# Performance work log

Measured on AMD Instinct MI355X. Metric: run time of the kernel, lower is better.

The kernel has to match this reference:

```python
import jax, jax.numpy as jnp
import numpy as np

HIDDEN = 2048
NUM_HEADS = 16
HEAD_DIM = HIDDEN // NUM_HEADS
BATCH, SEQ = 2, 2048


def setup_inputs() -> dict:
    key = jax.random.key(0)
    ks = jax.random.split(key, 9)
    s = 1.0 / np.sqrt(HIDDEN)
    return {
        "hidden_state": jax.random.normal(ks[0], (BATCH, SEQ, HIDDEN), dtype=jnp.float32),
        "Wq": jax.random.normal(ks[1], (HIDDEN, HIDDEN), dtype=jnp.float32) * s,
        "bq": jax.random.normal(ks[2], (HIDDEN,), dtype=jnp.float32) * 0.01,
        "Wk": jax.random.normal(ks[3], (HIDDEN, HIDDEN), dtype=jnp.float32) * s,
        "bk": jax.random.normal(ks[4], (HIDDEN,), dtype=jnp.float32) * 0.01,
        "Wv": jax.random.normal(ks[5], (HIDDEN, HIDDEN), dtype=jnp.float32) * s,
        "bv": jax.random.normal(ks[6], (HIDDEN,), dtype=jnp.float32) * 0.01,
        "Wo": jax.random.normal(ks[7], (HIDDEN, HIDDEN), dtype=jnp.float32) * s,
        "bo": jax.random.normal(ks[8], (HIDDEN,), dtype=jnp.float32) * 0.01,
    }


def _split_heads(x):
    # (B, S, H*D) -> (B, H, S, D)
    b, s, _ = x.shape
    return x.reshape(b, s, NUM_HEADS, HEAD_DIM).transpose(0, 2, 1, 3)


def reference(hidden_state, Wq, bq, Wk, bk, Wv, bv, Wo, bo):
    q = _split_heads(hidden_state @ Wq + bq)
    k = _split_heads(hidden_state @ Wk + bk)
    v = _split_heads(hidden_state @ Wv + bv)
    scale = 1.0 / jnp.sqrt(jnp.asarray(HEAD_DIM, dtype=hidden_state.dtype))
    scores = jnp.einsum("bhqd,bhkd->bhqk", q, k) * scale  # (B,H,S,S)
    probs = jax.nn.softmax(scores, axis=-1)
    out = jnp.einsum("bhqk,bhkd->bhqd", probs, v)  # (B,H,S,D)
    b, h, s, d = out.shape
    out = out.transpose(0, 2, 1, 3).reshape(b, s, h * d)  # merge heads
    return out @ Wo + bo
```

## Files before the change

### kernel.cpp

```cpp
#include <hip/hip_runtime.h>
#include <math.h>

typedef __bf16 bf16;
typedef __bf16 bf16x4 __attribute__((ext_vector_type(4)));
typedef __bf16 bf16x8 __attribute__((ext_vector_type(8)));
typedef float  f32x4  __attribute__((ext_vector_type(4)));

#define HIDDEN 2048
#define NH     16
#define HD     128
#define BATCH  2
#define SEQ    2048
#define MROWS  (BATCH*SEQ)
#define NQKV   (3*HIDDEN)

__device__ __forceinline__ void async16(const bf16* g, bf16* l) {
  __builtin_amdgcn_global_load_lds(
      (const __attribute__((address_space(1))) void*)g,
      (__attribute__((address_space(3))) void*)l, 16, 0, 0);
}

__global__ __launch_bounds__(256) void cast_f32_bf16_kernel(
    const float* __restrict__ src, bf16* __restrict__ dst, int n4) {
  int i = blockIdx.x * 256 + threadIdx.x;
  if (i >= n4) return;
  float4 f = ((const float4*)src)[i];
  bf16x4 o;
  o[0] = (bf16)f.x; o[1] = (bf16)f.y; o[2] = (bf16)f.z; o[3] = (bf16)f.w;
  ((bf16x4*)dst)[i] = o;
}

__global__ __launch_bounds__(256) void transpose_cast4_kernel(
    const float* __restrict__ s0, const float* __restrict__ s1,
    const float* __restrict__ s2, const float* __restrict__ s3,
    bf16* __restrict__ d0, bf16* __restrict__ d1,
    bf16* __restrict__ d2, bf16* __restrict__ d3) {
  const float* src; bf16* dst;
  switch (blockIdx.z) {
    case 0: src = s0; dst = d0; break;
    case 1: src = s1; dst = d1; break;
    case 2: src = s2; dst = d2; break;
    default: src = s3; dst = d3; break;
  }
  __shared__ float t[32][33];
  int x  = blockIdx.x * 32 + threadIdx.x;
  int y0 = blockIdx.y * 32;
#pragma unroll
  for (int i = 0; i < 32; i += 8)
    t[threadIdx.y + i][threadIdx.x] = src[(size_t)(y0 + threadIdx.y + i) * HIDDEN + x];
  __syncthreads();
  int xo  = blockIdx.y * 32 + threadIdx.x;
  int yo0 = blockIdx.x * 32;
#pragma unroll
  for (int i = 0; i < 32; i += 8)
    dst[(size_t)(yo0 + threadIdx.y + i) * HIDDEN + xo] = (bf16)t[threadIdx.x][threadIdx.y + i];
}

__global__ __launch_bounds__(256) void concat3_kernel(
    const float* __restrict__ a, const float* __restrict__ b,
    const float* __restrict__ c, float* __restrict__ dst) {
  int i = blockIdx.x * 256 + threadIdx.x;
  float v = (i < 2048) ? a[i] : (i < 4096 ? b[i - 2048] : c[i - 4096]);
  dst[i] = v;
}

__global__ __launch_bounds__(256) void transpose_v_kernel(
    const bf16* __restrict__ QKV, bf16* __restrict__ Vt) {
  __shared__ bf16 t[32][33];
  int bh = blockIdx.z, b = bh >> 4, h = bh & 15;
  const bf16* src = QKV + (size_t)b * SEQ * NQKV + 2 * HIDDEN + h * HD;
  bf16* dst = Vt + (size_t)bh * HD * SEQ;
  int s0 = blockIdx.x * 32, d0 = blockIdx.y * 32;
#pragma unroll
  for (int i = 0; i < 32; i += 8)
    t[threadIdx.y + i][threadIdx.x] = src[(size_t)(s0 + threadIdx.y + i) * NQKV + d0 + threadIdx.x];
  __syncthreads();
#pragma unroll
  for (int i = 0; i < 32; i += 8)
    dst[(size_t)(d0 + threadIdx.y + i) * SEQ + s0 + threadIdx.x] = t[threadIdx.x][threadIdx.y + i];
}

template <typename OutT>
__global__ __launch_bounds__(256) void gemm_bt_bias(
    const bf16* __restrict__ A, const bf16* __restrict__ Bt,
    const float* __restrict__ bias, OutT* __restrict__ C, int N, int K) {
  __shared__ bf16 Ash[128 * 32];
  __shared__ bf16 Bsh[128 * 32];
  const int tid = threadIdx.x;
  const int wave = tid >> 6, lane = tid & 63, quad = lane >> 4, l16 = lane & 15;
  const int wm = (wave & 1) * 64, wn = (wave >> 1) * 64;
  const int m0 = blockIdx.x * 128, n0 = blockIdx.y * 128;

  const f32x4 zero4 = {0.f, 0.f, 0.f, 0.f};
  f32x4 acc[4][4];
#pragma unroll
  for (int i = 0; i < 4; i++)
#pragma unroll
    for (int j = 0; j < 4; j++) acc[i][j] = zero4;

  const int crow = tid >> 2, ccc = tid & 3;
  const int cd = (ccc - (crow >> 1)) & 3;
  const int pc = (quad + (l16 >> 1)) & 3;

  for (int kt = 0; kt < K; kt += 32) {
    __syncthreads();
    async16(&A[(size_t)(m0 + crow) * K + kt + cd * 8],       &Ash[tid * 8]);
    async16(&A[(size_t)(m0 + crow + 64) * K + kt + cd * 8],  &Ash[2048 + tid * 8]);
    async16(&Bt[(size_t)(n0 + crow) * K + kt + cd * 8],      &Bsh[tid * 8]);
    async16(&Bt[(size_t)(n0 + crow + 64) * K + kt + cd * 8], &Bsh[2048 + tid * 8]);
    __syncthreads();

    bf16x8 af[4], bfr[4];
#pragma unroll
    for (int i = 0; i < 4; i++) af[i]  = *(const bf16x8*)&Ash[(wm + i * 16 + l16) * 32 + pc * 8];
#pragma unroll
    for (int j = 0; j < 4; j++) bfr[j] = *(const bf16x8*)&Bsh[(wn + j * 16 + l16) * 32 + pc * 8];
#pragma unroll
    for (int i = 0; i < 4; i++)
#pragma unroll
      for (int j = 0; j < 4; j++)
        acc[i][j] = __builtin_amdgcn_mfma_f32_16x16x32_bf16(af[i], bfr[j], acc[i][j], 0, 0, 0);
  }

#pragma unroll
  for (int i = 0; i < 4; i++)
#pragma unroll
    for (int j = 0; j < 4; j++) {
      int n = n0 + wn + j * 16 + l16;
      float bv = bias[n];
#pragma unroll
      for (int r = 0; r < 4; r++) {
        int m = m0 + wm + i * 16 + quad * 4 + r;
        C[(size_t)m * N + n] = (OutT)(acc[i][j][r] + bv);
      }
    }
}

#define KTS   64
#define PPAD  72

__global__ __launch_bounds__(256, 2) void flash_attn_kernel(
    const bf16* __restrict__ QKV, const bf16* __restrict__ Vt, bf16* __restrict__ O) {
  const int bh = blockIdx.y, b = bh >> 4, h = bh & 15;
  const int q0 = blockIdx.x * 128;
  const int tid = threadIdx.x, wave = tid >> 6, lane = tid & 63, quad = lane >> 4, l16 = lane & 15;

  const bf16* Qb  = QKV + (size_t)b * SEQ * NQKV + h * HD;
  const bf16* Kb  = QKV + (size_t)b * SEQ * NQKV + HIDDEN + h * HD;
  const bf16* Vtb = Vt + (size_t)bh * HD * SEQ;

  __shared__ bf16 Ksh[KTS * HD];
  __shared__ bf16 Vsh[HD * KTS];
  __shared__ bf16 Psh[128 * PPAD];

  const int qrow = q0 + wave * 32;
  const float sc = 0.08838834764831845f * 1.44269504088896340f;

  bf16x8 qf[2][4];
#pragma unroll
  for (int mt = 0; mt < 2; mt++)
#pragma unroll
    for (int kk = 0; kk < 4; kk++) {
      bf16x8 t = *(const bf16x8*)&Qb[(size_t)(qrow + mt * 16 + l16) * NQKV + kk * 32 + quad * 8];
#pragma unroll
      for (int j = 0; j < 8; j++) t[j] = (bf16)((float)t[j] * sc);
      qf[mt][kk] = t;
    }

  const f32x4 zero4 = {0.f, 0.f, 0.f, 0.f};
  f32x4 oacc[2][8];
#pragma unroll
  for (int mt = 0; mt < 2; mt++)
#pragma unroll
    for (int nt = 0; nt < 8; nt++) oacc[mt][nt] = zero4;

  float lrun[2][4];
#pragma unroll
  for (int mt = 0; mt < 2; mt++)
#pragma unroll
    for (int r = 0; r < 4; r++) lrun[mt][r] = 0.f;

  const int krp = tid >> 4, kpp = tid & 15;
  const int vrp = tid >> 3, vpp = tid & 7;
  const int l7 = l16 & 7;

  for (int kt = 0; kt < SEQ; kt += KTS) {
    __syncthreads();
#pragma unroll
    for (int s = 0; s < 4; s++) {
      int r  = s * 16 + krp;
      int c  = kpp ^ (r & 7);
      async16(&Kb[(size_t)(kt + r) * NQKV + c * 8], &Ksh[s * 2048 + tid * 8]);
      int rv = s * 32 + vrp;
      int cv = vpp ^ (rv & 7);
      async16(&Vtb[(size_t)rv * SEQ + kt + cv * 8], &Vsh[s * 2048 + tid * 8]);
    }
    __syncthreads();

    f32x4 sacc[2][4];
#pragma unroll
    for (int mt = 0; mt < 2; mt++)
#pragma unroll
      for (int nt = 0; nt < 4; nt++) sacc[mt][nt] = zero4;
#pragma unroll
    for (int kk = 0; kk < 4; kk++) {
      bf16x8 kf[4];
#pragma unroll
      for (int nt = 0; nt < 4; nt++) {
        int p = (4 * kk + quad) ^ l7;
        kf[nt] = *(const bf16x8*)&Ksh[(nt * 16 + l16) * HD + p * 8];
      }
#pragma unroll
      for (int mt = 0; mt < 2; mt++)
#pragma unroll
        for (int nt = 0; nt < 4; nt++)
          sacc[mt][nt] = __builtin_amdgcn_mfma_f32_16x16x32_bf16(qf[mt][kk], kf[nt], sacc[mt][nt], 0, 0, 0);
    }

    float rs[2][4] = {};
#pragma unroll
    for (int mt = 0; mt < 2; mt++)
#pragma unroll
      for (int nt = 0; nt < 4; nt++)
#pragma unroll
        for (int r = 0; r < 4; r++) {
          float p = exp2f(sacc[mt][nt][r]);
          rs[mt][r] += p;
          Psh[(wave * 32 + mt * 16 + quad * 4 + r) * PPAD + nt * 16 + l16] = (bf16)p;
        }
#pragma unroll
    for (int mt = 0; mt < 2; mt++)
#pragma unroll
      for (int r = 0; r < 4; r++) {
        float t = rs[mt][r];
        t += __shfl_xor(t, 1);
        t += __shfl_xor(t, 2);
        t += __shfl_xor(t, 4);
        t += __shfl_xor(t, 8);
        lrun[mt][r] += t;
      }

#pragma unroll
    for (int kk2 = 0; kk2 < 2; kk2++) {
      bf16x8 pf[2], vf[8];
#pragma unroll
      for (int mt = 0; mt < 2; mt++)
        pf[mt] = *(const bf16x8*)&Psh[(wave * 32 + mt * 16 + l16) * PPAD + kk2 * 32 + quad * 8];
#pragma unroll
      for (int nt = 0; nt < 8; nt++) {
        int p = (4 * kk2 + quad) ^ l7;
        vf[nt] = *(const bf16x8*)&Vsh[(nt * 16 + l16) * KTS + p * 8];
      }
#pragma unroll
      for (int mt = 0; mt < 2; mt++)
#pragma unroll
        for (int nt = 0; nt < 8; nt++)
          oacc[mt][nt] = __builtin_amdgcn_mfma_f32_16x16x32_bf16(pf[mt], vf[nt], oacc[mt][nt], 0, 0, 0);
    }
  }

#pragma unroll
  for (int mt = 0; mt < 2; mt++) {
    float inv[4];
#pragma unroll
    for (int r = 0; r < 4; r++) inv[r] = 1.0f / lrun[mt][r];
#pragma unroll
    for (int nt = 0; nt < 8; nt++)
#pragma unroll
      for (int r = 0; r < 4; r++) {
        int q = qrow + mt * 16 + quad * 4 + r;
        int d = nt * 16 + l16;
        O[(size_t)(b * SEQ + q) * HIDDEN + h * HD + d] = (bf16)(oacc[mt][nt][r] * inv[r]);
      }
  }
}

extern "C" void kernel_launch(void* const* d_in, const int* in_sizes, int n_in,
                              void* d_out, int out_size, void* d_ws, size_t ws_size,
                              hipStream_t stream) {
  const float* hs = (const float*)d_in[0];
  const float* Wq = (const float*)d_in[1];
  const float* bq = (const float*)d_in[2];
  const float* Wk = (const float*)d_in[3];
  const float* bk = (const float*)d_in[4];
  const float* Wv = (const float*)d_in[5];
  const float* bv = (const float*)d_in[6];
  const float* Wo = (const float*)d_in[7];
  const float* bo = (const float*)d_in[8];
  float* out = (float*)d_out;

  char* ws = (char*)d_ws;
  bf16*  Abf   = (bf16*)(ws);
  bf16*  WtQKV = (bf16*)(ws + 16777216);
  bf16*  WtO   = (bf16*)(ws + 41943040);
  float* biasQ = (float*)(ws + 50331648);
  bf16*  QKV   = (bf16*)(ws + 50356224);
  bf16*  VT    = (bf16*)(ws + 100687872);
  bf16*  Obf   = (bf16*)(ws + 117465088);

  dim3 tb(32, 8);
  cast_f32_bf16_kernel<<<8192, 256, 0, stream>>>(hs, Abf, 2097152);
  transpose_cast4_kernel<<<dim3(64, 64, 4), tb, 0, stream>>>(
      Wq, Wk, Wv, Wo,
      WtQKV, WtQKV + 2048 * 2048, WtQKV + 2 * 2048 * 2048, WtO);
  concat3_kernel<<<24, 256, 0, stream>>>(bq, bk, bv, biasQ);

  gemm_bt_bias<bf16><<<dim3(32, 48), 256, 0, stream>>>(Abf, WtQKV, biasQ, QKV, NQKV, HIDDEN);
  transpose_v_kernel<<<dim3(64, 4, 32), tb, 0, stream>>>(QKV, VT);
  flash_attn_kernel<<<dim3(16, 32), 256, 0, stream>>>(QKV, VT, Obf);
  gemm_bt_bias<float><<<dim3(32, 16), 256, 0, stream>>>(Obf, WtO, bo, out, HIDDEN, HIDDEN);
}
```

Before: 464.0 us.

## Deepen GEMM K-tile to 64 and transpose score MFMA in attention

The projection GEMM now stages 64-wide K tiles in shared memory with an 8-way swizzle, which halves the number of barrier pairs per output tile and hoists address computation into incremented pointers. The attention kernel swaps the MFMA operands so each lane holds one query row's scores. That lets P be written as packed bf16x4 stores, and the row-sum reduction needs two cross-lane shuffles instead of four per row. The final normalisation gathers row sums with a shuffle. Doubled LDS per GEMM block may reduce occupancy.

```diff
diff --git a/kernel.cpp b/kernel.cpp
--- a/kernel.cpp
+++ b/kernel.cpp
@@ -84,8 +84,8 @@
 __global__ __launch_bounds__(256) void gemm_bt_bias(
     const bf16* __restrict__ A, const bf16* __restrict__ Bt,
     const float* __restrict__ bias, OutT* __restrict__ C, int N, int K) {
-  __shared__ bf16 Ash[128 * 32];
-  __shared__ bf16 Bsh[128 * 32];
+  __shared__ bf16 Ash[128 * 64];
+  __shared__ bf16 Bsh[128 * 64];
   const int tid = threadIdx.x;
   const int wave = tid >> 6, lane = tid & 63, quad = lane >> 4, l16 = lane & 15;
   const int wm = (wave & 1) * 64, wn = (wave >> 1) * 64;
@@ -98,28 +98,42 @@
 #pragma unroll
     for (int j = 0; j < 4; j++) acc[i][j] = zero4;
 
-  const int crow = tid >> 2, ccc = tid & 3;
-  const int cd = (ccc - (crow >> 1)) & 3;
-  const int pc = (quad + (l16 >> 1)) & 3;
-
-  for (int kt = 0; kt < K; kt += 32) {
+  const int crow = tid >> 3, ccc = tid & 7;
+  const int cd = (ccc - crow) & 7;
+  const int l7 = l16 & 7;
+
+  const bf16* pa[4];
+  const bf16* pb[4];
+#pragma unroll
+  for (int s = 0; s < 4; s++) {
+    pa[s] = &A[(size_t)(m0 + s * 32 + crow) * K + cd * 8];
+    pb[s] = &Bt[(size_t)(n0 + s * 32 + crow) * K + cd * 8];
+  }
+
+  for (int kt = 0; kt < K; kt += 64) {
     __syncthreads();
-    async16(&A[(size_t)(m0 + crow) * K + kt + cd * 8],       &Ash[tid * 8]);
-    async16(&A[(size_t)(m0 + crow + 64) * K + kt + cd * 8],  &Ash[2048 + tid * 8]);
-    async16(&Bt[(size_t)(n0 + crow) * K + kt + cd * 8],      &Bsh[tid * 8]);
-    async16(&Bt[(size_t)(n0 + crow + 64) * K + kt + cd * 8], &Bsh[2048 + tid * 8]);
+#pragma unroll
+    for (int s = 0; s < 4; s++) {
+      async16(pa[s], &Ash[s * 2048 + tid * 8]);
+      async16(pb[s], &Bsh[s * 2048 + tid * 8]);
+      pa[s] += 64; pb[s] += 64;
+    }
     __syncthreads();
 
-    bf16x8 af[4], bfr[4];
-#pragma unroll
-    for (int i = 0; i < 4; i++) af[i]  = *(const bf16x8*)&Ash[(wm + i * 16 + l16) * 32 + pc * 8];
-#pragma unroll
-    for (int j = 0; j < 4; j++) bfr[j] = *(const bf16x8*)&Bsh[(wn + j * 16 + l16) * 32 + pc * 8];
-#pragma unroll
-    for (int i = 0; i < 4; i++)
-#pragma unroll
-      for (int j = 0; j < 4; j++)
-        acc[i][j] = __builtin_amdgcn_mfma_f32_16x16x32_bf16(af[i], bfr[j], acc[i][j], 0, 0, 0);
+#pragma unroll
+    for (int kk = 0; kk < 2; kk++) {
+      const int pc = (kk * 4 + quad + l7) & 7;
+      bf16x8 af[4], bfr[4];
+#pragma unroll
+      for (int i = 0; i < 4; i++) af[i]  = *(const bf16x8*)&Ash[(wm + i * 16 + l16) * 64 + pc * 8];
+#pragma unroll
+      for (int j = 0; j < 4; j++) bfr[j] = *(const bf16x8*)&Bsh[(wn + j * 16 + l16) * 64 + pc * 8];
+#pragma unroll
+      for (int i = 0; i < 4; i++)
+#pragma unroll
+        for (int j = 0; j < 4; j++)
+          acc[i][j] = __builtin_amdgcn_mfma_f32_16x16x32_bf16(af[i], bfr[j], acc[i][j], 0, 0, 0);
+    }
   }
 
 #pragma unroll
@@ -174,71 +188,73 @@
 #pragma unroll
     for (int nt = 0; nt < 8; nt++) oacc[mt][nt] = zero4;
 
-  float lrun[2][4];
-#pragma unroll
-  for (int mt = 0; mt < 2; mt++)
-#pragma unroll
-    for (int r = 0; r < 4; r++) lrun[mt][r] = 0.f;
+  float lrun[2] = {0.f, 0.f};
 
   const int krp = tid >> 4, kpp = tid & 15;
   const int vrp = tid >> 3, vpp = tid & 7;
   const int l7 = l16 & 7;
 
+  const bf16* pk[4];
+  const bf16* pv[4];
+#pragma unroll
+  for (int s = 0; s < 4; s++) {
+    int r  = s * 16 + krp;
+    pk[s] = &Kb[(size_t)r * NQKV + (kpp ^ (r & 7)) * 8];
+    int rv = s * 32 + vrp;
+    pv[s] = &Vtb[(size_t)rv * SEQ + (vpp ^ (rv & 7)) * 8];
+  }
+
   for (int kt = 0; kt < SEQ; kt += KTS) {
     __syncthreads();
 #pragma unroll
     for (int s = 0; s < 4; s++) {
-      int r  = s * 16 + krp;
-      int c  = kpp ^ (r & 7);
-      async16(&Kb[(size_t)(kt + r) * NQKV + c * 8], &Ksh[s * 2048 + tid * 8]);
-      int rv = s * 32 + vrp;
-      int cv = vpp ^ (rv & 7);
-      async16(&Vtb[(size_t)rv * SEQ + kt + cv * 8], &Vsh[s * 2048 + tid * 8]);
+      async16(pk[s], &Ksh[s * 2048 + tid * 8]);
+      async16(pv[s], &Vsh[s * 2048 + tid * 8]);
+      pk[s] += (size_t)KTS * NQKV;
+      pv[s] += KTS;
     }
     __syncthreads();
 
-    f32x4 sacc[2][4];
+    f32x4 st[2][4];
 #pragma unroll
     for (int mt = 0; mt < 2; mt++)
 #pragma unroll
-      for (int nt = 0; nt < 4; nt++) sacc[mt][nt] = zero4;
+      for (int nt = 0; nt < 4; nt++) st[mt][nt] = zero4;
 #pragma unroll
     for (int kk = 0; kk < 4; kk++) {
+      const int p = (4 * kk + quad) ^ l7;
       bf16x8 kf[4];
 #pragma unroll
+      for (int nt = 0; nt < 4; nt++)
+        kf[nt] = *(const bf16x8*)&Ksh[(nt * 16 + l16) * HD + p * 8];
+#pragma unroll
+      for (int mt = 0; mt < 2; mt++)
+#pragma unroll
+        for (int nt = 0; nt < 4; nt++)
+          st[mt][nt] = __builtin_amdgcn_mfma_f32_16x16x32_bf16(kf[nt], qf[mt][kk], st[mt][nt], 0, 0, 0);
+    }
+
+    float rs[2] = {0.f, 0.f};
+#pragma unroll
+    for (int mt = 0; mt < 2; mt++)
+#pragma unroll
       for (int nt = 0; nt < 4; nt++) {
-        int p = (4 * kk + quad) ^ l7;
-        kf[nt] = *(const bf16x8*)&Ksh[(nt * 16 + l16) * HD + p * 8];
+        bf16x4 pk4;
+#pragma unroll
+        for (int r = 0; r < 4; r++) {
+          float p = exp2f(st[mt][nt][r]);
+          rs[mt] += p;
+          pk4[r] = (bf16)p;
+        }
+        *(bf16x4*)&Psh[(wave * 32 + mt * 16 + l16) * PPAD + nt * 16 + quad * 4] = pk4;
       }
 #pragma unroll
-      for (int mt = 0; mt < 2; mt++)
-#pragma unroll
-        for (int nt = 0; nt < 4; nt++)
-          sacc[mt][nt] = __builtin_amdgcn_mfma_f32_16x16x32_bf16(qf[mt][kk], kf[nt], sacc[mt][nt], 0, 0, 0);
-    }
-
-    float rs[2][4] = {};
-#pragma unroll
-    for (int mt = 0; mt < 2; mt++)
-#pragma unroll
-      for (int nt = 0; nt < 4; nt++)
-#pragma unroll
-        for (int r = 0; r < 4; r++) {
-          float p = exp2f(sacc[mt][nt][r]);
-          rs[mt][r] += p;
-          Psh[(wave * 32 + mt * 16 + quad * 4 + r) * PPAD + nt * 16 + l16] = (bf16)p;
-        }
-#pragma unroll
-    for (int mt = 0; mt < 2; mt++)
-#pragma unroll
-      for (int r = 0; r < 4; r++) {
-        float t = rs[mt][r];
-        t += __shfl_xor(t, 1);
-        t += __shfl_xor(t, 2);
-        t += __shfl_xor(t, 4);
-        t += __shfl_xor(t, 8);
-        lrun[mt][r] += t;
-      }
+    for (int mt = 0; mt < 2; mt++) {
+      float t = rs[mt];
+      t += __shfl_xor(t, 16);
+      t += __shfl_xor(t, 32);
+      lrun[mt] += t;
+    }
 
 #pragma unroll
     for (int kk2 = 0; kk2 < 2; kk2++) {
@@ -263,7 +279,8 @@
   for (int mt = 0; mt < 2; mt++) {
     float inv[4];
 #pragma unroll
-    for (int r = 0; r < 4; r++) inv[r] = 1.0f / lrun[mt][r];
+    for (int r = 0; r < 4; r++)
+      inv[r] = 1.0f / __shfl(lrun[mt], (lane & 48) | (quad * 4 + r));
 #pragma unroll
     for (int nt = 0; nt < 8; nt++)
 #pragma unroll
```

New measurement: 408.2 us. 1.14x faster.
